# Optimization experiments

Measured on AMD Instinct MI355X. Metric: run time of the kernel, lower is better.

Reference implementation:

```python
import jax, jax.numpy as jnp
import numpy as np

B, S = 2, 1024          # 2 sequences of 1024 tokens (prefill)
HID = 2880
HQ, HKV, D = 64, 8, 64  # query heads, kv heads, head_dim
W = 128                 # sliding window size
THETA = 150000.0
SCALE = D ** -0.5
Q_SIZE, KV_SIZE = HQ * D, HKV * D


def _rope_neox(pos, x):
    # pos: [T] int, x: [T, H, D] -> neox-style full-dim rotary
    half = D // 2
    inv_freq = 1.0 / (THETA ** (jnp.arange(half, dtype=jnp.float32) * 2.0 / D))
    ang = pos.astype(jnp.float32)[:, None] * inv_freq          # [T, D/2]
    cos = jnp.cos(ang)[:, None, :]                             # [T, 1, D/2]
    sin = jnp.sin(ang)[:, None, :]
    x1, x2 = x[..., :half], x[..., half:]
    return jnp.concatenate([x1 * cos - x2 * sin, x1 * sin + x2 * cos], axis=-1)


def setup_inputs() -> dict:
    key = jax.random.key(0)
    ks = jax.random.split(key, 10)
    s = 0.02
    hidden_states = jax.random.normal(ks[0], (B * S, HID), dtype=jnp.float32)
    positions = jnp.tile(jnp.arange(S, dtype=jnp.int32), B)    # per-sequence positions
    Wq = jax.random.normal(ks[1], (HID, Q_SIZE), dtype=jnp.float32) * s
    bq = jax.random.normal(ks[2], (Q_SIZE,), dtype=jnp.float32) * s
    Wk = jax.random.normal(ks[3], (HID, KV_SIZE), dtype=jnp.float32) * s
    bk = jax.random.normal(ks[4], (KV_SIZE,), dtype=jnp.float32) * s
    Wv = jax.random.normal(ks[5], (HID, KV_SIZE), dtype=jnp.float32) * s
    bv = jax.random.normal(ks[6], (KV_SIZE,), dtype=jnp.float32) * s
    Wo = jax.random.normal(ks[7], (Q_SIZE, HID), dtype=jnp.float32) * s
    bo = jax.random.normal(ks[8], (HID,), dtype=jnp.float32) * s
    return {"hidden_states": hidden_states, "positions": positions,
            "Wq": Wq, "bq": bq, "Wk": Wk, "bk": bk,
            "Wv": Wv, "bv": bv, "Wo": Wo, "bo": bo}


def reference(hidden_states, positions, Wq, bq, Wk, bk, Wv, bv, Wo, bo):
    T = hidden_states.shape[0]
    q = (hidden_states @ Wq + bq).reshape(T, HQ, D)
    k = (hidden_states @ Wk + bk).reshape(T, HKV, D)
    v = (hidden_states @ Wv + bv).reshape(T, HKV, D)
    q = _rope_neox(positions, q)
    k = _rope_neox(positions, k)

    # sliding-window causal attention (banded, window = last W keys + self)
    G = HQ // HKV  # GQA group size
    q5 = q.reshape(B, S, HKV, G, D)
    k4 = k.reshape(B, S, HKV, D)
    v4 = v.reshape(B, S, HKV, D)
    offs = jnp.arange(W + 1)
    idx = jnp.arange(S)[:, None] - W + offs[None, :]           # [S, W+1] key index j
    valid = idx >= 0                                           # causal+window band
    idx_c = jnp.clip(idx, 0, S - 1)
    kw = k4[:, idx_c]                                          # [B, S, W+1, HKV, D]
    vw = v4[:, idx_c]
    scores = jnp.einsum('bikgd,biwkd->bikgw', q5, kw) * SCALE  # [B,S,HKV,G,W+1]
    scores = jnp.where(valid[None, :, None, None, :], scores, jnp.float32(-1e30))
    p = jax.nn.softmax(scores, axis=-1)
    o = jnp.einsum('bikgw,biwkd->bikgd', p, vw).reshape(T, Q_SIZE)
    return o @ Wo + bo


if __name__ == '__main__':
    out = reference(**setup_inputs())
    print(out.shape, out.dtype)
```

## Files before the change

kernel.cpp:

```cpp
#include <hip/hip_runtime.h>

#define T_TOK 2048
#define S_LEN 1024
#define HIDN  2880
#define NHQ   64
#define NHKV  8
#define DH    64
#define QSZ   4096
#define KVSZ  512
#define WIN   128
#define NQKV  5120
#define NOPAD 2944

typedef __attribute__((ext_vector_type(4))) float f32x4;
typedef __attribute__((ext_vector_type(8))) short bf16x8;
typedef __attribute__((ext_vector_type(4))) short s16x4;

__device__ __forceinline__ unsigned short f2bf(float f) {
  unsigned u = __float_as_uint(f);
  u += 0x7fffu + ((u >> 16) & 1u);
  return (unsigned short)(u >> 16);
}
__device__ __forceinline__ float bf2f(unsigned short s) {
  return __uint_as_float(((unsigned)s) << 16);
}
__device__ __forceinline__ void ld_g2l16(const void* g, void* l) {
  __builtin_amdgcn_global_load_lds(
      (const __attribute__((address_space(1))) unsigned int*)g,
      (__attribute__((address_space(3))) unsigned int*)l, 16, 0, 0);
}

__global__ __launch_bounds__(256) void convert_hidden(
    const float* __restrict__ in, unsigned short* __restrict__ out)
{
  const size_t off = ((size_t)blockIdx.x * 256 + threadIdx.x) * 8;
  const f32x4 a = *(const f32x4*)(in + off);
  const f32x4 b = *(const f32x4*)(in + off + 4);
  bf16x8 p;
  p[0] = (short)f2bf(a[0]); p[1] = (short)f2bf(a[1]);
  p[2] = (short)f2bf(a[2]); p[3] = (short)f2bf(a[3]);
  p[4] = (short)f2bf(b[0]); p[5] = (short)f2bf(b[1]);
  p[6] = (short)f2bf(b[2]); p[7] = (short)f2bf(b[3]);
  *(bf16x8*)(out + off) = p;
}

__global__ __launch_bounds__(256) void transpose_w(
    const float* __restrict__ W, unsigned short* __restrict__ WT,
    int K, int N)
{
  __shared__ float tile[32][72];
  const int tid = threadIdx.x;
  const int nb = blockIdx.x * 64;
  const int kb = blockIdx.y * 32;
  const int kk = tid >> 3;
  const int n8 = (tid & 7) * 8;
  if (nb + 64 <= N) {
    const float* src = W + (size_t)(kb + kk) * N + nb + n8;
    *(f32x4*)&tile[kk][n8]     = *(const f32x4*)(src);
    *(f32x4*)&tile[kk][n8 + 4] = *(const f32x4*)(src + 4);
  } else {
    #pragma unroll
    for (int u = 0; u < 8; ++u)
      tile[kk][n8 + u] = (nb + n8 + u < N)
          ? W[(size_t)(kb + kk) * N + nb + n8 + u] : 0.f;
  }
  __syncthreads();
  const int n  = tid & 63;
  const int k8 = (tid >> 6) * 8;
  bf16x8 p;
  #pragma unroll
  for (int j = 0; j < 8; ++j) p[j] = (short)f2bf(tile[k8 + j][n]);
  *(bf16x8*)(WT + (size_t)(nb + n) * K + kb + k8) = p;
}

__device__ __forceinline__ void gemm_core(
    const unsigned short* __restrict__ A, const unsigned short* __restrict__ BT,
    int K, int m0, int n0, unsigned short* As, unsigned short* Bs,
    f32x4 acc[4][4])
{
  const int tid  = threadIdx.x;
  const int lane = tid & 63;
  const int wid  = tid >> 6;
  const int wm = (wid >> 1) * 64;
  const int wn = (wid & 1) * 64;
  const int fr = lane & 15;
  const int fq = lane >> 4;

  const int rsub = tid >> 3;
  const int cg   = (tid & 7) ^ (rsub & 7);
  const unsigned short* Ap = A  + (size_t)(m0 + rsub) * K + cg * 8;
  const unsigned short* Bp = BT + (size_t)(n0 + rsub) * K + cg * 8;
  const size_t rstep = (size_t)32 * K;

  for (int k0 = 0; k0 < K; k0 += 64) {
    #pragma unroll
    for (int i = 0; i < 4; ++i) {
      ld_g2l16(Ap + i * rstep + k0, As + ((size_t)i * 256 + tid) * 8);
      ld_g2l16(Bp + i * rstep + k0, Bs + ((size_t)i * 256 + tid) * 8);
    }
    __syncthreads();
    #pragma unroll
    for (int ks = 0; ks < 2; ++ks) {
      const int kc = ks * 4 + fq;
      bf16x8 af[4], bfr[4];
      #pragma unroll
      for (int mt = 0; mt < 4; ++mt) {
        const int R = wm + mt * 16 + fr;
        af[mt] = *(const bf16x8*)(As + R * 64 + ((kc ^ (R & 7)) << 3));
      }
      #pragma unroll
      for (int nt = 0; nt < 4; ++nt) {
        const int R = wn + nt * 16 + fr;
        bfr[nt] = *(const bf16x8*)(Bs + R * 64 + ((kc ^ (R & 7)) << 3));
      }
      #pragma unroll
      for (int mt = 0; mt < 4; ++mt)
        #pragma unroll
        for (int nt = 0; nt < 4; ++nt)
          acc[mt][nt] = __builtin_amdgcn_mfma_f32_16x16x32_bf16(
              af[mt], bfr[nt], acc[mt][nt], 0, 0, 0);
    }
    __syncthreads();
  }
}

__device__ __forceinline__ void rope_epilogue(
    f32x4 acc[4][4], const float* __restrict__ bias,
    const int* __restrict__ pos, unsigned short* __restrict__ outp,
    int outStride, int colbase, int rowbase, int lane)
{
  const int fr = lane & 15;
  const int r4 = (lane >> 4) * 4;
  const float invf0 = exp2f((float)fr        * (-17.19460283f / 32.0f));
  const float invf1 = exp2f((float)(fr + 16) * (-17.19460283f / 32.0f));
  #pragma unroll
  for (int mt = 0; mt < 4; ++mt) {
    #pragma unroll
    for (int i = 0; i < 4; ++i) {
      const int m = rowbase + mt * 16 + r4 + i;
      const float p = (float)pos[m];
      #pragma unroll
      for (int ntp = 0; ntp < 2; ++ntp) {
        float sv, cv;
        __sincosf(p * (ntp ? invf1 : invf0), &sv, &cv);
        const int c1 = colbase + ntp * 16 + fr;
        const float x1 = acc[mt][ntp][i]     + bias[c1];
        const float x2 = acc[mt][ntp + 2][i] + bias[c1 + 32];
        outp[(size_t)m * outStride + c1]      = f2bf(x1 * cv - x2 * sv);
        outp[(size_t)m * outStride + c1 + 32] = f2bf(x1 * sv + x2 * cv);
      }
    }
  }
}

__global__ __launch_bounds__(256) void gemm_qkv(
    const unsigned short* __restrict__ A, const unsigned short* __restrict__ BT,
    const float* __restrict__ bq, const float* __restrict__ bk,
    const float* __restrict__ bv, const int* __restrict__ pos,
    unsigned short* __restrict__ qb, unsigned short* __restrict__ kb,
    unsigned short* __restrict__ vT)
{
  __shared__ unsigned short As[128 * 64];
  __shared__ unsigned short Bs[128 * 64];
  const int m0 = blockIdx.y * 128;
  const int n0 = blockIdx.x * 128;
  f32x4 acc[4][4];
  #pragma unroll
  for (int i = 0; i < 4; ++i)
    #pragma unroll
    for (int j = 0; j < 4; ++j) acc[i][j] = (f32x4){0.f, 0.f, 0.f, 0.f};
  gemm_core(A, BT, HIDN, m0, n0, As, Bs, acc);

  const int lane = threadIdx.x & 63;
  const int wid  = threadIdx.x >> 6;
  const int wm = (wid >> 1) * 64;
  const int wn = (wid & 1) * 64;
  const int fr = lane & 15;
  const int r4 = (lane >> 4) * 4;

  if (n0 < QSZ) {
    rope_epilogue(acc, bq, pos, qb, QSZ, n0 + wn, m0 + wm, lane);
  } else if (n0 < QSZ + KVSZ) {
    rope_epilogue(acc, bk, pos, kb, KVSZ, n0 - QSZ + wn, m0 + wm, lane);
  } else {
    #pragma unroll
    for (int nt = 0; nt < 4; ++nt) {
      const int vrow = n0 - (QSZ + KVSZ) + wn + nt * 16 + fr;
      const float bvv = bv[vrow];
      #pragma unroll
      for (int mt = 0; mt < 4; ++mt) {
        const int mb = m0 + wm + mt * 16 + r4;
        s16x4 p;
        p[0] = (short)f2bf(acc[mt][nt][0] + bvv);
        p[1] = (short)f2bf(acc[mt][nt][1] + bvv);
        p[2] = (short)f2bf(acc[mt][nt][2] + bvv);
        p[3] = (short)f2bf(acc[mt][nt][3] + bvv);
        *(s16x4*)(vT + (size_t)vrow * T_TOK + mb) = p;
      }
    }
  }
}

__global__ __launch_bounds__(128) void gemm_o(
    const unsigned short* __restrict__ A, const unsigned short* __restrict__ BT,
    const float* __restrict__ bias, float* __restrict__ C)
{
  __shared__ unsigned short As[64 * 64];
  __shared__ unsigned short Bs[128 * 64];
  const int tid  = threadIdx.x;
  const int lane = tid & 63;
  const int wid  = tid >> 6;
  const int m0 = blockIdx.y * 64;
  const int n0 = blockIdx.x * 128;
  const int wn = wid * 64;
  const int fr = lane & 15;
  const int fq = lane >> 4;

  f32x4 acc[4][4];
  #pragma unroll
  for (int i = 0; i < 4; ++i)
    #pragma unroll
    for (int j = 0; j < 4; ++j) acc[i][j] = (f32x4){0.f, 0.f, 0.f, 0.f};

  const int rsub = tid >> 3;
  const int cg   = (tid & 7) ^ (rsub & 7);
  const unsigned short* Ap = A  + (size_t)(m0 + rsub) * QSZ + cg * 8;
  const unsigned short* Bp = BT + (size_t)(n0 + rsub) * QSZ + cg * 8;
  const size_t rstep = (size_t)16 * QSZ;

  for (int k0 = 0; k0 < QSZ; k0 += 64) {
    #pragma unroll
    for (int i = 0; i < 4; ++i)
      ld_g2l16(Ap + i * rstep + k0, As + ((size_t)i * 128 + tid) * 8);
    #pragma unroll
    for (int i = 0; i < 8; ++i)
      ld_g2l16(Bp + i * rstep + k0, Bs + ((size_t)i * 128 + tid) * 8);
    __syncthreads();
    #pragma unroll
    for (int ks = 0; ks < 2; ++ks) {
      const int kc = ks * 4 + fq;
      bf16x8 af[4], bfr[4];
      #pragma unroll
      for (int mt = 0; mt < 4; ++mt) {
        const int R = mt * 16 + fr;
        af[mt] = *(const bf16x8*)(As + R * 64 + ((kc ^ (R & 7)) << 3));
      }
      #pragma unroll
      for (int nt = 0; nt < 4; ++nt) {
        const int R = wn + nt * 16 + fr;
        bfr[nt] = *(const bf16x8*)(Bs + R * 64 + ((kc ^ (R & 7)) << 3));
      }
      #pragma unroll
      for (int mt = 0; mt < 4; ++mt)
        #pragma unroll
        for (int nt = 0; nt < 4; ++nt)
          acc[mt][nt] = __builtin_amdgcn_mfma_f32_16x16x32_bf16(
              af[mt], bfr[nt], acc[mt][nt], 0, 0, 0);
    }
    __syncthreads();
  }

  const int r4 = (lane >> 4) * 4;
  #pragma unroll
  for (int nt = 0; nt < 4; ++nt) {
    const int n = n0 + wn + nt * 16 + fr;
    if (n >= HIDN) continue;
    const float bvv = bias[n];
    #pragma unroll
    for (int mt = 0; mt < 4; ++mt) {
      const int mb = m0 + mt * 16 + r4;
      #pragma unroll
      for (int i = 0; i < 4; ++i)
        C[(size_t)(mb + i) * HIDN + n] = acc[mt][nt][i] + bvv;
    }
  }
}

__global__ __launch_bounds__(256, 3) void attn_kernel(
    const unsigned short* __restrict__ q, const unsigned short* __restrict__ k,
    const unsigned short* __restrict__ vT, unsigned short* __restrict__ o)
{
  __shared__ unsigned short lds[26624];
  unsigned short* Ks = lds;
  unsigned short* Vt = lds;
  unsigned short* Ps = lds + 13824;

  const int tid  = threadIdx.x;
  const int lane = tid & 63;
  const int wid  = tid >> 6;
  const int sq0  = blockIdx.x * 64;
  const int hp   = blockIdx.y;
  const int b    = blockIdx.z;
  const int h0   = hp * 2;
  const int kvh  = hp >> 2;
  const int kp0  = sq0 - WIN;

  const int fr = lane & 15;
  const int fk = (lane >> 4) * 8;
  const int qw = wid * 16;

  bf16x8 qf[2][2];
  {
    const size_t qrow = (size_t)(b * S_LEN + sq0 + qw + fr) * QSZ;
    #pragma unroll
    for (int hh = 0; hh < 2; ++hh)
      #pragma unroll
      for (int ks2 = 0; ks2 < 2; ++ks2)
        qf[hh][ks2] = *(const bf16x8*)(q + qrow + (h0 + hh) * DH + ks2 * 32 + fk);
  }

  #pragma unroll
  for (int j = 0; j < 6; ++j) {
    const int c  = tid + j * 256;
    const int kr = c >> 3, dc = (c & 7) * 8;
    int tok = b * S_LEN + kp0 + kr;
    if (tok < 0) tok = 0;
    const bf16x8 vv = *(const bf16x8*)(k + (size_t)tok * KVSZ + kvh * DH + dc);
    *(bf16x8*)&Ks[kr * 72 + dc] = vv;
  }
  __syncthreads();

  f32x4 S0[12], S1[12];
  #pragma unroll
  for (int i = 0; i < 12; ++i) {
    S0[i] = (f32x4){0.f, 0.f, 0.f, 0.f};
    S1[i] = (f32x4){0.f, 0.f, 0.f, 0.f};
  }
  #pragma unroll
  for (int ks2 = 0; ks2 < 2; ++ks2) {
    #pragma unroll
    for (int nt = 0; nt < 12; ++nt) {
      const bf16x8 bfr = *(const bf16x8*)&Ks[(nt * 16 + fr) * 72 + ks2 * 32 + fk];
      S0[nt] = __builtin_amdgcn_mfma_f32_16x16x32_bf16(qf[0][ks2], bfr, S0[nt], 0, 0, 0);
      S1[nt] = __builtin_amdgcn_mfma_f32_16x16x32_bf16(qf[1][ks2], bfr, S1[nt], 0, 0, 0);
    }
  }

  const int qbase = sq0 + qw + ((lane >> 4) << 2);
  float ls0[4] = {0.f, 0.f, 0.f, 0.f};
  float ls1[4] = {0.f, 0.f, 0.f, 0.f};
  #pragma unroll
  for (int nt = 0; nt < 12; ++nt) {
    const int jpos = kp0 + nt * 16 + fr;
    #pragma unroll
    for (int i = 0; i < 4; ++i) {
      const int qa = qbase + i;
      const bool valid = (jpos >= 0) && (jpos <= qa) && (jpos >= qa - WIN);
      const float e0 = valid ? __expf(S0[nt][i] * 0.125f) : 0.f;
      const float e1 = valid ? __expf(S1[nt][i] * 0.125f) : 0.f;
      S0[nt][i] = e0; ls0[i] += e0;
      S1[nt][i] = e1; ls1[i] += e1;
    }
  }
  #pragma unroll
  for (int off = 1; off < 16; off <<= 1)
    #pragma unroll
    for (int i = 0; i < 4; ++i) {
      ls0[i] += __shfl_xor(ls0[i], off, 64);
      ls1[i] += __shfl_xor(ls1[i], off, 64);
    }
  float inv0[4], inv1[4];
  #pragma unroll
  for (int i = 0; i < 4; ++i) {
    inv0[i] = 1.0f / ls0[i];
    inv1[i] = 1.0f / ls1[i];
  }
  __syncthreads();

  #pragma unroll
  for (int nt = 0; nt < 12; ++nt)
    #pragma unroll
    for (int i = 0; i < 4; ++i)
      Ps[(qbase - sq0 + i) * 200 + nt * 16 + fr] = f2bf(S0[nt][i]);
  if (kp0 >= 0) {
    #pragma unroll
    for (int j = 0; j < 6; ++j) {
      const int c  = tid + j * 256;
      const int dr = c / 24, kc = (c % 24) * 8;
      const bf16x8 vv = *(const bf16x8*)(
          vT + (size_t)(kvh * DH + dr) * T_TOK + b * S_LEN + kp0 + kc);
      *(bf16x8*)&Vt[dr * 200 + kc] = vv;
    }
  } else {
    #pragma unroll
    for (int j = 0; j < 6; ++j) {
      const int c  = tid + j * 256;
      const int dr = c / 24, kc = (c % 24) * 8;
      bf16x8 vv;
      #pragma unroll
      for (int u = 0; u < 8; ++u) {
        int col = b * S_LEN + kp0 + kc + u;
        if (col < 0) col = 0;
        vv[u] = (short)vT[(size_t)(kvh * DH + dr) * T_TOK + col];
      }
      *(bf16x8*)&Vt[dr * 200 + kc] = vv;
    }
  }
  __syncthreads();

  {
    f32x4 O[4];
    #pragma unroll
    for (int i = 0; i < 4; ++i) O[i] = (f32x4){0.f, 0.f, 0.f, 0.f};
    #pragma unroll
    for (int ks2 = 0; ks2 < 6; ++ks2) {
      const bf16x8 pa = *(const bf16x8*)&Ps[(qw + fr) * 200 + ks2 * 32 + fk];
      #pragma unroll
      for (int nt = 0; nt < 4; ++nt) {
        const bf16x8 vb = *(const bf16x8*)&Vt[(nt * 16 + fr) * 200 + ks2 * 32 + fk];
        O[nt] = __builtin_amdgcn_mfma_f32_16x16x32_bf16(pa, vb, O[nt], 0, 0, 0);
      }
    }
    #pragma unroll
    for (int nt = 0; nt < 4; ++nt)
      #pragma unroll
      for (int i = 0; i < 4; ++i)
        o[(size_t)(b * S_LEN + qbase + i) * QSZ + h0 * DH + nt * 16 + fr] =
            f2bf(O[nt][i] * inv0[i]);
  }
  __syncthreads();

  #pragma unroll
  for (int nt = 0; nt < 12; ++nt)
    #pragma unroll
    for (int i = 0; i < 4; ++i)
      Ps[(qbase - sq0 + i) * 200 + nt * 16 + fr] = f2bf(S1[nt][i]);
  __syncthreads();

  {
    f32x4 O[4];
    #pragma unroll
    for (int i = 0; i < 4; ++i) O[i] = (f32x4){0.f, 0.f, 0.f, 0.f};
    #pragma unroll
    for (int ks2 = 0; ks2 < 6; ++ks2) {
      const bf16x8 pa = *(const bf16x8*)&Ps[(qw + fr) * 200 + ks2 * 32 + fk];
      #pragma unroll
      for (int nt = 0; nt < 4; ++nt) {
        const bf16x8 vb = *(const bf16x8*)&Vt[(nt * 16 + fr) * 200 + ks2 * 32 + fk];
        O[nt] = __builtin_amdgcn_mfma_f32_16x16x32_bf16(pa, vb, O[nt], 0, 0, 0);
      }
    }
    #pragma unroll
    for (int nt = 0; nt < 4; ++nt)
      #pragma unroll
      for (int i = 0; i < 4; ++i)
        o[(size_t)(b * S_LEN + qbase + i) * QSZ + (h0 + 1) * DH + nt * 16 + fr] =
            f2bf(O[nt][i] * inv1[i]);
  }
}

extern "C" void kernel_launch(void* const* d_in, const int* in_sizes, int n_in,
                              void* d_out, int out_size, void* d_ws, size_t ws_size,
                              hipStream_t stream) {
  const float* hidden    = (const float*)d_in[0];
  const int*   positions = (const int*)d_in[1];
  const float* Wq = (const float*)d_in[2];
  const float* bq = (const float*)d_in[3];
  const float* Wk = (const float*)d_in[4];
  const float* bk = (const float*)d_in[5];
  const float* Wv = (const float*)d_in[6];
  const float* bv = (const float*)d_in[7];
  const float* Wo = (const float*)d_in[8];
  const float* bo = (const float*)d_in[9];
  float* out = (float*)d_out;

  char* ws = (char*)d_ws;
  unsigned short* hbf   = (unsigned short*)(ws);
  unsigned short* WqkvT = (unsigned short*)(ws + 11796480);
  unsigned short* qb    = (unsigned short*)(ws + 41287680);
  unsigned short* kb    = (unsigned short*)(ws + 58064896);
  unsigned short* vTb   = (unsigned short*)(ws + 60162048);

  const dim3 blk(256);
  convert_hidden<<<dim3((T_TOK * HIDN) / 2048), blk, 0, stream>>>(hidden, hbf);
  transpose_w<<<dim3(QSZ / 64, HIDN / 32), blk, 0, stream>>>(
      Wq, WqkvT, HIDN, QSZ);
  transpose_w<<<dim3(KVSZ / 64, HIDN / 32), blk, 0, stream>>>(
      Wk, WqkvT + (size_t)QSZ * HIDN, HIDN, KVSZ);
  transpose_w<<<dim3(KVSZ / 64, HIDN / 32), blk, 0, stream>>>(
      Wv, WqkvT + (size_t)(QSZ + KVSZ) * HIDN, HIDN, KVSZ);

  gemm_qkv<<<dim3(NQKV / 128, T_TOK / 128), blk, 0, stream>>>(
      hbf, WqkvT, bq, bk, bv, positions, qb, kb, vTb);

  transpose_w<<<dim3(NOPAD / 64, QSZ / 32), blk, 0, stream>>>(
      Wo, WqkvT, QSZ, HIDN);

  attn_kernel<<<dim3(S_LEN / 64, NHQ / 2, 2), blk, 0, stream>>>(
      qb, kb, vTb, qb);
  gemm_o<<<dim3(NOPAD / 128, T_TOK / 64), dim3(128), 0, stream>>>(
      qb, WqkvT, bo, out);
}
```

Baseline: 396.5 us.

## Merge prep kernels into one launch and shrink QKV GEMM tile to 64x128

The hidden-state conversion and the three Wq/Wk/Wv transpose launches become a single prep kernel that dispatches on block index, removing three launches and their tail gaps. The QKV GEMM moves from 128x128 tiles with 256 threads to 64x128 tiles with 128 threads, doubling the block count from 640 to 1280 for better CU fill. The cost is lower data reuse per block and more B-tile reloads.

After: 385.4 us. 2.8% less time.

```diff
diff --git a/kernel.cpp b/kernel.cpp
--- a/kernel.cpp
+++ b/kernel.cpp
@@ -30,18 +30,58 @@
       (__attribute__((address_space(3))) unsigned int*)l, 16, 0, 0);
 }
 
-__global__ __launch_bounds__(256) void convert_hidden(
-    const float* __restrict__ in, unsigned short* __restrict__ out)
-{
-  const size_t off = ((size_t)blockIdx.x * 256 + threadIdx.x) * 8;
-  const f32x4 a = *(const f32x4*)(in + off);
-  const f32x4 b = *(const f32x4*)(in + off + 4);
+#define NB_CONV 2880
+#define NB_WQ   5760
+#define NB_WK   720
+
+__device__ __forceinline__ void transpose_tile(
+    const float* __restrict__ W, unsigned short* __restrict__ WT,
+    int N, int lbid, float (*tile)[72])
+{
+  const int tid = threadIdx.x;
+  const int nbx = N >> 6;
+  const int nb = (lbid % nbx) * 64;
+  const int kb = (lbid / nbx) * 32;
+  const int kk = tid >> 3;
+  const int n8 = (tid & 7) * 8;
+  const float* src = W + (size_t)(kb + kk) * N + nb + n8;
+  *(f32x4*)&tile[kk][n8]     = *(const f32x4*)(src);
+  *(f32x4*)&tile[kk][n8 + 4] = *(const f32x4*)(src + 4);
+  __syncthreads();
+  const int n  = tid & 63;
+  const int k8 = (tid >> 6) * 8;
   bf16x8 p;
-  p[0] = (short)f2bf(a[0]); p[1] = (short)f2bf(a[1]);
-  p[2] = (short)f2bf(a[2]); p[3] = (short)f2bf(a[3]);
-  p[4] = (short)f2bf(b[0]); p[5] = (short)f2bf(b[1]);
-  p[6] = (short)f2bf(b[2]); p[7] = (short)f2bf(b[3]);
-  *(bf16x8*)(out + off) = p;
+  #pragma unroll
+  for (int j = 0; j < 8; ++j) p[j] = (short)f2bf(tile[k8 + j][n]);
+  *(bf16x8*)(WT + (size_t)(nb + n) * HIDN + kb + k8) = p;
+}
+
+__global__ __launch_bounds__(256) void prep_kernel(
+    const float* __restrict__ hidden, unsigned short* __restrict__ hbf,
+    const float* __restrict__ Wq, const float* __restrict__ Wk,
+    const float* __restrict__ Wv, unsigned short* __restrict__ WT)
+{
+  __shared__ float tile[32][72];
+  const int bid = blockIdx.x;
+  if (bid < NB_CONV) {
+    const size_t off = ((size_t)bid * 256 + threadIdx.x) * 8;
+    const f32x4 a = *(const f32x4*)(hidden + off);
+    const f32x4 b = *(const f32x4*)(hidden + off + 4);
+    bf16x8 p;
+    p[0] = (short)f2bf(a[0]); p[1] = (short)f2bf(a[1]);
+    p[2] = (short)f2bf(a[2]); p[3] = (short)f2bf(a[3]);
+    p[4] = (short)f2bf(b[0]); p[5] = (short)f2bf(b[1]);
+    p[6] = (short)f2bf(b[2]); p[7] = (short)f2bf(b[3]);
+    *(bf16x8*)(hbf + off) = p;
+  } else if (bid < NB_CONV + NB_WQ) {
+    transpose_tile(Wq, WT, QSZ, bid - NB_CONV, tile);
+  } else if (bid < NB_CONV + NB_WQ + NB_WK) {
+    transpose_tile(Wk, WT + (size_t)QSZ * HIDN, KVSZ,
+                   bid - NB_CONV - NB_WQ, tile);
+  } else {
+    transpose_tile(Wv, WT + (size_t)(QSZ + KVSZ) * HIDN, KVSZ,
+                   bid - NB_CONV - NB_WQ - NB_WK, tile);
+  }
 }
 
 __global__ __launch_bounds__(256) void transpose_w(
@@ -73,57 +113,6 @@
   *(bf16x8*)(WT + (size_t)(nb + n) * K + kb + k8) = p;
 }
 
-__device__ __forceinline__ void gemm_core(
-    const unsigned short* __restrict__ A, const unsigned short* __restrict__ BT,
-    int K, int m0, int n0, unsigned short* As, unsigned short* Bs,
-    f32x4 acc[4][4])
-{
-  const int tid  = threadIdx.x;
-  const int lane = tid & 63;
-  const int wid  = tid >> 6;
-  const int wm = (wid >> 1) * 64;
-  const int wn = (wid & 1) * 64;
-  const int fr = lane & 15;
-  const int fq = lane >> 4;
-
-  const int rsub = tid >> 3;
-  const int cg   = (tid & 7) ^ (rsub & 7);
-  const unsigned short* Ap = A  + (size_t)(m0 + rsub) * K + cg * 8;
-  const unsigned short* Bp = BT + (size_t)(n0 + rsub) * K + cg * 8;
-  const size_t rstep = (size_t)32 * K;
-
-  for (int k0 = 0; k0 < K; k0 += 64) {
-    #pragma unroll
-    for (int i = 0; i < 4; ++i) {
-      ld_g2l16(Ap + i * rstep + k0, As + ((size_t)i * 256 + tid) * 8);
-      ld_g2l16(Bp + i * rstep + k0, Bs + ((size_t)i * 256 + tid) * 8);
-    }
-    __syncthreads();
-    #pragma unroll
-    for (int ks = 0; ks < 2; ++ks) {
-      const int kc = ks * 4 + fq;
-      bf16x8 af[4], bfr[4];
-      #pragma unroll
-      for (int mt = 0; mt < 4; ++mt) {
-        const int R = wm + mt * 16 + fr;
-        af[mt] = *(const bf16x8*)(As + R * 64 + ((kc ^ (R & 7)) << 3));
-      }
-      #pragma unroll
-      for (int nt = 0; nt < 4; ++nt) {
-        const int R = wn + nt * 16 + fr;
-        bfr[nt] = *(const bf16x8*)(Bs + R * 64 + ((kc ^ (R & 7)) << 3));
-      }
-      #pragma unroll
-      for (int mt = 0; mt < 4; ++mt)
-        #pragma unroll
-        for (int nt = 0; nt < 4; ++nt)
-          acc[mt][nt] = __builtin_amdgcn_mfma_f32_16x16x32_bf16(
-              af[mt], bfr[nt], acc[mt][nt], 0, 0, 0);
-    }
-    __syncthreads();
-  }
-}
-
 __device__ __forceinline__ void rope_epilogue(
     f32x4 acc[4][4], const float* __restrict__ bias,
     const int* __restrict__ pos, unsigned short* __restrict__ outp,
@@ -153,35 +142,73 @@
   }
 }
 
-__global__ __launch_bounds__(256) void gemm_qkv(
+__global__ __launch_bounds__(128) void gemm_qkv(
     const unsigned short* __restrict__ A, const unsigned short* __restrict__ BT,
     const float* __restrict__ bq, const float* __restrict__ bk,
     const float* __restrict__ bv, const int* __restrict__ pos,
     unsigned short* __restrict__ qb, unsigned short* __restrict__ kb,
     unsigned short* __restrict__ vT)
 {
-  __shared__ unsigned short As[128 * 64];
+  __shared__ unsigned short As[64 * 64];
   __shared__ unsigned short Bs[128 * 64];
-  const int m0 = blockIdx.y * 128;
+  const int tid  = threadIdx.x;
+  const int lane = tid & 63;
+  const int wid  = tid >> 6;
+  const int m0 = blockIdx.y * 64;
   const int n0 = blockIdx.x * 128;
+  const int wn = wid * 64;
+  const int fr = lane & 15;
+  const int fq = lane >> 4;
+
   f32x4 acc[4][4];
   #pragma unroll
   for (int i = 0; i < 4; ++i)
     #pragma unroll
     for (int j = 0; j < 4; ++j) acc[i][j] = (f32x4){0.f, 0.f, 0.f, 0.f};
-  gemm_core(A, BT, HIDN, m0, n0, As, Bs, acc);
-
-  const int lane = threadIdx.x & 63;
-  const int wid  = threadIdx.x >> 6;
-  const int wm = (wid >> 1) * 64;
-  const int wn = (wid & 1) * 64;
-  const int fr = lane & 15;
+
+  const int rsub = tid >> 3;
+  const int cg   = (tid & 7) ^ (rsub & 7);
+  const unsigned short* Ap = A  + (size_t)(m0 + rsub) * HIDN + cg * 8;
+  const unsigned short* Bp = BT + (size_t)(n0 + rsub) * HIDN + cg * 8;
+  const size_t rstep = (size_t)16 * HIDN;
+
+  for (int k0 = 0; k0 < HIDN; k0 += 64) {
+    #pragma unroll
+    for (int i = 0; i < 4; ++i)
+      ld_g2l16(Ap + i * rstep + k0, As + ((size_t)i * 128 + tid) * 8);
+    #pragma unroll
+    for (int i = 0; i < 8; ++i)
+      ld_g2l16(Bp + i * rstep + k0, Bs + ((size_t)i * 128 + tid) * 8);
+    __syncthreads();
+    #pragma unroll
+    for (int ks = 0; ks < 2; ++ks) {
+      const int kc = ks * 4 + fq;
+      bf16x8 af[4], bfr[4];
+      #pragma unroll
+      for (int mt = 0; mt < 4; ++mt) {
+        const int R = mt * 16 + fr;
+        af[mt] = *(const bf16x8*)(As + R * 64 + ((kc ^ (R & 7)) << 3));
+      }
+      #pragma unroll
+      for (int nt = 0; nt < 4; ++nt) {
+        const int R = wn + nt * 16 + fr;
+        bfr[nt] = *(const bf16x8*)(Bs + R * 64 + ((kc ^ (R & 7)) << 3));
+      }
+      #pragma unroll
+      for (int mt = 0; mt < 4; ++mt)
+        #pragma unroll
+        for (int nt = 0; nt < 4; ++nt)
+          acc[mt][nt] = __builtin_amdgcn_mfma_f32_16x16x32_bf16(
+              af[mt], bfr[nt], acc[mt][nt], 0, 0, 0);
+    }
+    __syncthreads();
+  }
+
   const int r4 = (lane >> 4) * 4;
-
   if (n0 < QSZ) {
-    rope_epilogue(acc, bq, pos, qb, QSZ, n0 + wn, m0 + wm, lane);
+    rope_epilogue(acc, bq, pos, qb, QSZ, n0 + wn, m0, lane);
   } else if (n0 < QSZ + KVSZ) {
-    rope_epilogue(acc, bk, pos, kb, KVSZ, n0 - QSZ + wn, m0 + wm, lane);
+    rope_epilogue(acc, bk, pos, kb, KVSZ, n0 - QSZ + wn, m0, lane);
   } else {
     #pragma unroll
     for (int nt = 0; nt < 4; ++nt) {
@@ -189,7 +216,7 @@
       const float bvv = bv[vrow];
       #pragma unroll
       for (int mt = 0; mt < 4; ++mt) {
-        const int mb = m0 + wm + mt * 16 + r4;
+        const int mb = m0 + mt * 16 + r4;
         s16x4 p;
         p[0] = (short)f2bf(acc[mt][nt][0] + bvv);
         p[1] = (short)f2bf(acc[mt][nt][1] + bvv);
@@ -471,22 +498,16 @@
   unsigned short* kb    = (unsigned short*)(ws + 58064896);
   unsigned short* vTb   = (unsigned short*)(ws + 60162048);
 
-  const dim3 blk(256);
-  convert_hidden<<<dim3((T_TOK * HIDN) / 2048), blk, 0, stream>>>(hidden, hbf);
-  transpose_w<<<dim3(QSZ / 64, HIDN / 32), blk, 0, stream>>>(
-      Wq, WqkvT, HIDN, QSZ);
-  transpose_w<<<dim3(KVSZ / 64, HIDN / 32), blk, 0, stream>>>(
-      Wk, WqkvT + (size_t)QSZ * HIDN, HIDN, KVSZ);
-  transpose_w<<<dim3(KVSZ / 64, HIDN / 32), blk, 0, stream>>>(
-      Wv, WqkvT + (size_t)(QSZ + KVSZ) * HIDN, HIDN, KVSZ);
-
-  gemm_qkv<<<dim3(NQKV / 128, T_TOK / 128), blk, 0, stream>>>(
+  prep_kernel<<<dim3(NB_CONV + NB_WQ + 2 * NB_WK), dim3(256), 0, stream>>>(
+      hidden, hbf, Wq, Wk, Wv, WqkvT);
+
+  gemm_qkv<<<dim3(NQKV / 128, T_TOK / 64), dim3(128), 0, stream>>>(
       hbf, WqkvT, bq, bk, bv, positions, qb, kb, vTb);
 
-  transpose_w<<<dim3(NOPAD / 64, QSZ / 32), blk, 0, stream>>>(
+  transpose_w<<<dim3(NOPAD / 64, QSZ / 32), dim3(256), 0, stream>>>(
       Wo, WqkvT, QSZ, HIDN);
 
-  attn_kernel<<<dim3(S_LEN / 64, NHQ / 2, 2), blk, 0, stream>>>(
+  attn_kernel<<<dim3(S_LEN / 64, NHQ / 2, 2), dim3(256), 0, stream>>>(
       qb, kb, vTb, qb);
   gemm_o<<<dim3(NOPAD / 128, T_TOK / 64), dim3(128), 0, stream>>>(
       qb, WqkvT, bo, out);
```
